# Optimization experiments

Hardware: AMD Instinct MI355X
Metric: run time of the kernel (lower is better)

Reference implementation:

```python
import jax, jax.numpy as jnp
import numpy as np

B_SZ, SEQ, CH, ORDER = 8, 8192, 256, 64
EPS_LN = 1e-5
EPS_H = 1e-6


def setup_inputs() -> dict:
    key = jax.random.key(0)
    ks = jax.random.split(key, 12)
    s = 1.0 / np.sqrt(CH)
    x = jax.random.normal(ks[0], (B_SZ, SEQ, CH), jnp.float32)
    # RTF params: A = denominator coeffs (monic, leading 1 implied), B = numerator coeffs
    A = 0.01 * jax.random.normal(ks[1], (CH, ORDER), jnp.float32)  # small -> stable 1/A(z)
    Bp = 0.1 * jax.random.normal(ks[2], (CH, ORDER), jnp.float32)
    h0 = jnp.zeros((1,), jnp.float32)  # init torch.tensor([0.])
    W_enc = s * jax.random.normal(ks[3], (CH, CH), jnp.float32)
    b_enc = jnp.zeros((CH,), jnp.float32)
    W_fc = s * jax.random.normal(ks[4], (CH, CH), jnp.float32)
    b_fc = jnp.zeros((CH,), jnp.float32)
    gamma = jnp.ones((CH,), jnp.float32)
    beta = jnp.zeros((CH,), jnp.float32)
    W_dec = s * jax.random.normal(ks[5], (CH, CH), jnp.float32)
    b_dec = jnp.zeros((CH,), jnp.float32)
    return {"x": x, "A": A, "Bp": Bp, "h0": h0, "W_enc": W_enc, "b_enc": b_enc,
            "W_fc": W_fc, "b_fc": b_fc, "gamma": gamma, "beta": beta,
            "W_dec": W_dec, "b_dec": b_dec}


def _rtf_kernel(A, Bp, L):
    # K(z) = B(z)/A(z) with monic denominator a = [1, A_1..A_order]
    C = A.shape[0]
    a = jnp.concatenate([jnp.ones((C, 1), A.dtype), A], axis=1)  # (C, order+1)
    af = jnp.fft.rfft(a, n=L, axis=1)
    bf = jnp.fft.rfft(Bp, n=L, axis=1)
    return jnp.fft.irfft(bf / af, n=L, axis=1)  # (C, L)


def _causal_fft_conv(x, K):
    # x: (B, L, C); K: (C, L) per-channel causal filter
    L = x.shape[1]
    n = 2 * L
    xf = jnp.fft.rfft(x, n=n, axis=1)            # (B, n/2+1, C)
    Kf = jnp.fft.rfft(K.T, n=n, axis=0)          # (n/2+1, C)
    return jnp.fft.irfft(xf * Kf[None], n=n, axis=1)[:, :L]


def reference(x, A, Bp, h0, W_enc, b_enc, W_fc, b_fc, gamma, beta, W_dec, b_dec):
    gelu = lambda t: jax.nn.gelu(t, approximate=False)
    xe = x @ W_enc.T + b_enc                      # encode
    L = xe.shape[1]
    K = _rtf_kernel(A, Bp, L)                     # kernel generation from (A,B)
    h1 = _causal_fft_conv(xe, K)                  # FFT long convolution
    y1 = gelu(h1 + h0 * xe)                       # SSMRTF output (mult_activation=gelu)
    y2 = gelu(y1 @ W_fc.T + b_fc)                 # fc + final_act
    y2 = y2 + xe                                  # skip
    mu = jnp.mean(y2, axis=-1, keepdims=True)     # LayerNorm over channels
    var = jnp.mean(jnp.square(y2 - mu), axis=-1, keepdims=True)
    y2 = (y2 - mu) * jax.lax.rsqrt(var + EPS_LN) * gamma + beta
    y = y2 @ W_dec.T + b_dec                      # decode
    # h = ||y||_inf over seq / ||x_enc||_inf over seq
    h = jnp.max(jnp.abs(y), axis=1) / (jnp.max(jnp.abs(xe), axis=1) + EPS_H)
    return (y, h)
```

## Files before the change

### kernel.cpp

```cpp
#include <hip/hip_runtime.h>
#include <math.h>


#define BSZ   8
#define SEQ   8192
#define CHN   256
#define ORD   64
#define STAPS 512
#define NDD   17
#define PREPAD 544
#define XROW  (PREPAD + SEQ)
#define MTOT  (BSZ * SEQ)
#define YELEMS (MTOT * CHN)

#define CT2   1024
#define CTP   1032
#define CROW2 2048

typedef short s16x8 __attribute__((ext_vector_type(8)));
typedef float f32x4 __attribute__((ext_vector_type(4)));

#define MFMA16(a, b, c) __builtin_amdgcn_mfma_f32_16x16x32_bf16((a), (b), (c), 0, 0, 0)

__device__ __forceinline__ void gll16(const void* g, void* l) {
  __builtin_amdgcn_global_load_lds(
      (const __attribute__((address_space(1))) unsigned int*)g,
      (__attribute__((address_space(3))) unsigned int*)l, 16, 0, 0);
}

#define PERMC(row, h) (((row) * 8 + ((h) ^ ((row) & 7))) * 8)

__device__ __forceinline__ unsigned short f2bf(float f) {
  unsigned u = __float_as_uint(f);
  return (unsigned short)((u + 0x7FFFu + ((u >> 16) & 1u)) >> 16);
}
__device__ __forceinline__ float bf2f(unsigned short h) {
  return __uint_as_float(((unsigned)h) << 16);
}
__device__ __forceinline__ float geluf(float x) {
  float x2 = x * x;
  float y = x * __builtin_fmaf(0.0356774081f, x2, 0.7978845608f);
  float e = __builtin_amdgcn_exp2f(-2.8853900818f * y);
  return x * __builtin_amdgcn_rcpf(1.0f + e);
}
__device__ __forceinline__ uint4 packbf8(float4 a, float4 b) {
  uint4 r;
  r.x = (unsigned)f2bf(a.x) | ((unsigned)f2bf(a.y) << 16);
  r.y = (unsigned)f2bf(a.z) | ((unsigned)f2bf(a.w) << 16);
  r.z = (unsigned)f2bf(b.x) | ((unsigned)f2bf(b.y) << 16);
  r.w = (unsigned)f2bf(b.z) | ((unsigned)f2bf(b.w) << 16);
  return r;
}

__device__ __forceinline__ void kgen8(float* smemk, const float* A, const float* Bp,
                                      unsigned short* afr, int blk) {
  int tid = threadIdx.x, lane = tid & 63, wv = tid >> 6;
  int c = blk * 8 + wv;
  float* base = smemk + wv * 1872;
  float* G0 = base;
  float* G1 = base + 584;
  float* Et = base + 1168;
  float* Asl = base + 1232;
  float* Bsl = base + 1296;
  float* Kb = base + 1360;

  Asl[lane] = A[(size_t)c * ORD + lane];
  Bsl[lane] = Bp[(size_t)c * ORD + lane];
  for (int i = lane; i < 1168; i += 64) base[i] = 0.f;
  if (lane == 0) { G0[64] = 1.f; G1[65] = 1.f; }

  for (int n = 1; n < STAPS; n <<= 1) {
    int par = (n + lane) & 1;
    const float* Gc = par ? G1 : G0;
    int I0 = 64 + n + lane + par;
    float e0 = 0.f, e1 = 0.f, e2 = 0.f, e3 = 0.f;
#pragma unroll
    for (int g = 0; g < 16; ++g) {
      float4 av = *(const float4*)&Asl[4 * g];
      float2 vA = *(const float2*)&Gc[I0 - 4 * g - 2];
      float2 vB = *(const float2*)&Gc[I0 - 4 * g - 4];
      e0 += av.x * vA.y;
      e1 += av.y * vA.x;
      e2 += av.z * vB.y;
      e3 += av.w * vB.x;
    }
    Et[lane] = (e0 + e1) + (e2 + e3);
    int nk = (n + 63) >> 6;
    for (int k = 0; k < nk; ++k) {
      int idx = k * 64 + lane;
      int parU = (idx + 1) & 1;
      const float* Gu = parU ? G1 : G0;
      int J0 = 64 + idx - 1 + parU;
      float a0 = 0.f, a1 = 0.f, a2 = 0.f, a3 = 0.f;
#pragma unroll
      for (int g = 0; g < 16; ++g) {
        float4 ev = *(const float4*)&Et[4 * g];
        float2 vA = *(const float2*)&Gu[J0 - 4 * g];
        float2 vB = *(const float2*)&Gu[J0 - 4 * g - 2];
        a0 += ev.x * vA.y;
        a1 += ev.y * vA.x;
        a2 += ev.z * vB.y;
        a3 += ev.w * vB.x;
      }
      if (idx < n) {
        float gv = -((a0 + a1) + (a2 + a3));
        G0[64 + n + idx] = gv;
        G1[65 + n + idx] = gv;
      }
    }
  }

  for (int k = 0; k < 8; ++k) {
    int t = k * 64 + lane;
    int parB = (t + 1) & 1;
    const float* Gb = parB ? G1 : G0;
    int J0 = 64 + t - 1 + parB;
    float a0 = 0.f, a1 = 0.f, a2 = 0.f, a3 = 0.f;
#pragma unroll
    for (int g = 0; g < 16; ++g) {
      float4 bv = *(const float4*)&Bsl[4 * g];
      float2 vA = *(const float2*)&Gb[J0 - 4 * g];
      float2 vB = *(const float2*)&Gb[J0 - 4 * g - 2];
      a0 += bv.x * vA.y;
      a1 += bv.y * vA.x;
      a2 += bv.z * vB.y;
      a3 += bv.w * vB.x;
    }
    Kb[t] = (a0 + a1) + (a2 + a3);
  }

  int m = lane & 15, quad = lane >> 4;
  for (int dd = 0; dd < NDD; ++dd) {
    unsigned short v[8];
#pragma unroll
    for (int j = 0; j < 8; ++j) {
      int k = quad * 8 + j;
      int d = 2 * dd + (k >> 4);
      int p = k & 15;
      int s = 16 * d + m - p;
      float kv = (s >= 0 && s < STAPS) ? Kb[s] : 0.f;
      v[j] = f2bf(kv);
    }
    uint4 pk;
    pk.x = (unsigned)v[0] | ((unsigned)v[1] << 16);
    pk.y = (unsigned)v[2] | ((unsigned)v[3] << 16);
    pk.z = (unsigned)v[4] | ((unsigned)v[5] << 16);
    pk.w = (unsigned)v[6] | ((unsigned)v[7] << 16);
    *(uint4*)(afr + ((size_t)(c * NDD + dd) * 64 + lane) * 8) = pk;
  }
}

__global__ __launch_bounds__(512) void k_pzk(const float* A, const float* Bp,
                                             unsigned short* afr,
                                             const float* we, const float* wf,
                                             const float* wd, unsigned short* owe,
                                             unsigned short* owf, unsigned short* owd,
                                             unsigned short* xeT, uint4* maxbufs) {
  __shared__ __align__(16) float smemk[8 * 1872];
  int bx = blockIdx.x, tid = threadIdx.x;
  if (bx < 32) {
    kgen8(smemk, A, Bp, afr, bx);
    return;
  }
  int i = (bx - 32) * 512 + tid;
  if (i < 196608) {
    int which = i >> 16, off = i & 65535;
    if (which == 0)      owe[off] = f2bf(we[off]);
    else if (which == 1) owf[off] = f2bf(wf[off]);
    else                 owd[off] = f2bf(wd[off]);
  } else {
    int j = i - 196608;
    uint4 z; z.x = 0; z.y = 0; z.z = 0; z.w = 0;
    if (j < 139264) {
      int row = j / 68, cc = j % 68;
      *(uint4*)((char*)xeT + (size_t)row * (XROW * 2) + (size_t)cc * 16) = z;
    } else {
      maxbufs[j - 139264] = z;
    }
  }
}

__global__ __launch_bounds__(256) void k_gemm1(const float* x, const unsigned short* wb,
                                               const float* benc, unsigned short* xeT,
                                               unsigned int* maxxe) {
  __shared__ __align__(16) char smem[40960];
  unsigned short* As = (unsigned short*)smem;
  unsigned short* Bs = (unsigned short*)(smem + 32768);
  int tid = threadIdx.x, lane = tid & 63, wv = tid >> 6;
  int ln15 = lane & 15, hf = lane >> 4;
  size_t t0 = (size_t)blockIdx.x * 64;
  int b = (int)(t0 >> 13), tin = (int)(t0 & 8191);
  f32x4 acc[4][4];
#pragma unroll
  for (int i = 0; i < 4; ++i)
#pragma unroll
    for (int j = 0; j < 4; ++j) { acc[i][j][0]=0.f; acc[i][j][1]=0.f; acc[i][j][2]=0.f; acc[i][j][3]=0.f; }

  for (int k0 = 0; k0 < CHN; k0 += 64) {
    __syncthreads();
#pragma unroll
    for (int i = 0; i < 8; ++i) {
      int p = 512 * wv + 64 * i + lane;
      int row = p >> 3, h = (p & 7) ^ (row & 7);
      gll16(wb + (size_t)row * CHN + k0 + h * 8, &As[(512 * wv + 64 * i) * 8]);
    }
    {
      int row = tid >> 2, hb = (tid & 3) * 2;
      const float* src = x + (t0 + row) * CHN + k0 + hb * 8;
      float4 f0 = *(const float4*)src;
      float4 f1 = *(const float4*)(src + 4);
      float4 f2 = *(const float4*)(src + 8);
      float4 f3 = *(const float4*)(src + 12);
      *(uint4*)&Bs[PERMC(row, hb)]     = packbf8(f0, f1);
      *(uint4*)&Bs[PERMC(row, hb + 1)] = packbf8(f2, f3);
    }
    __syncthreads();
#pragma unroll
    for (int ks = 0; ks < 2; ++ks) {
      s16x8 af[4], bfr[4];
#pragma unroll
      for (int mt = 0; mt < 4; ++mt) {
        int row = 64 * wv + 16 * mt + ln15;
        af[mt] = *(const s16x8*)&As[PERMC(row, ks * 4 + hf)];
      }
#pragma unroll
      for (int nt = 0; nt < 4; ++nt) {
        int row = 16 * nt + ln15;
        bfr[nt] = *(const s16x8*)&Bs[PERMC(row, ks * 4 + hf)];
      }
#pragma unroll
      for (int mt = 0; mt < 4; ++mt)
#pragma unroll
        for (int nt = 0; nt < 4; ++nt)
          acc[mt][nt] = MFMA16(af[mt], bfr[nt], acc[mt][nt]);
    }
  }
  int quad = hf;
  unsigned short* bb = (unsigned short*)smem;
  __syncthreads();
#pragma unroll
  for (int mt = 0; mt < 4; ++mt) {
#pragma unroll
    for (int r = 0; r < 4; ++r) {
      int row = 64 * wv + 16 * mt + 4 * quad + r;
      float bias = benc[row];
      float mv = 0.f;
#pragma unroll
      for (int nt = 0; nt < 4; ++nt) {
        float v = acc[mt][nt][r] + bias;
        bb[row * 68 + 16 * nt + ln15] = f2bf(v);
        mv = fmaxf(mv, fabsf(v));
      }
      mv = fmaxf(mv, __shfl_xor(mv, 1)); mv = fmaxf(mv, __shfl_xor(mv, 2));
      mv = fmaxf(mv, __shfl_xor(mv, 4)); mv = fmaxf(mv, __shfl_xor(mv, 8));
      if (ln15 == 0) atomicMax(&maxxe[b * CHN + row], __float_as_uint(mv));
    }
  }
  __syncthreads();
  {
    int rbase = wv * 4 + quad;
#pragma unroll
    for (int it = 0; it < 16; ++it) {
      int row = it * 16 + rbase;
      uint2 val = *(const uint2*)&bb[row * 68 + ln15 * 4];
      *(uint2*)(xeT + (size_t)(b * CHN + row) * XROW + PREPAD + tin + ln15 * 4) = val;
    }
  }
}

__global__ __launch_bounds__(512) void k_conv(const unsigned short* xeT,
                                              const unsigned short* afr,
                                              unsigned short* y1, const float* h0p) {
  __shared__ __align__(16) unsigned short xet[8 * CROW2];
  __shared__ __align__(16) unsigned short bnc[8 * CTP];
  int tid = threadIdx.x, lane = tid & 63, wv = tid >> 6;
  int idx = blockIdx.x;
  int tg = idx & 7, cg = (idx >> 3) & 31, b = idx >> 8;
  int c0 = cg * 8, t0 = tg * CT2;
  int c = c0 + wv;

  s16x8 afrg[NDD];
  {
    const unsigned short* ap = afr + (size_t)c * (NDD * 512) + (size_t)lane * 8;
#pragma unroll
    for (int dd = 0; dd < NDD; ++dd)
      afrg[dd] = *(const s16x8*)(ap + (size_t)dd * 512);
  }
  {
    int lp = lane ^ ((lane >> 3) & 7);
    const unsigned short* gbase = xeT + (size_t)(b * CHN + c) * XROW + t0;
    unsigned short* lbase = &xet[wv * CROW2];
#pragma unroll
    for (int k = 0; k < 4; ++k)
      gll16(gbase + (size_t)(64 * k + lp) * 8, &lbase[k * 64 * 8]);
  }
  float h0 = h0p[0];

  int n = lane & 15, quad = lane >> 4;
  int qc = quad - ((quad >> 1) << 2);
  const char* xb = (const char*)&xet[wv * CROW2];

  int ad[NDD];
  {
    int cb0 = 2 * n + qc + 68;
#pragma unroll
    for (int dd = 0; dd < NDD; ++dd) {
      int cc = cb0 - 4 * dd;
      ad[dd] = (cc ^ ((cc >> 3) & 7)) * 16;
    }
  }
  int ead;
  {
    int ch = 68 + 2 * n + (quad >> 1);
    ead = (ch ^ ((ch >> 3) & 7)) * 16 + 8 * (quad & 1);
  }
  __syncthreads();

#pragma unroll 1
  for (int s = 0; s < 4; ++s) {
    f32x4 a0, a1;
    a0[0]=0.f; a0[1]=0.f; a0[2]=0.f; a0[3]=0.f;
    a1[0]=0.f; a1[1]=0.f; a1[2]=0.f; a1[3]=0.f;
#pragma unroll
    for (int dd = 0; dd < 16; dd += 2) {
      a0 = MFMA16(afrg[dd],     *(const s16x8*)(xb + ad[dd]),     a0);
      a1 = MFMA16(afrg[dd + 1], *(const s16x8*)(xb + ad[dd + 1]), a1);
    }
    a0 = MFMA16(afrg[16], *(const s16x8*)(xb + ad[16]), a0);
    uint2 xvp = *(const uint2*)(xb + ead);
    unsigned short o[4];
#pragma unroll
    for (int r = 0; r < 4; ++r) {
      float xv = bf2f(((const unsigned short*)&xvp)[r]);
      float v = (a0[r] + a1[r]) + h0 * xv;
      o[r] = f2bf(geluf(v));
    }
    uint2 pw;
    pw.x = (unsigned)o[0] | ((unsigned)o[1] << 16);
    pw.y = (unsigned)o[2] | ((unsigned)o[3] << 16);
    *(uint2*)&bnc[wv * CTP + 256 * s + 16 * n + 4 * quad] = pw;
#pragma unroll
    for (int dd = 16; dd >= 8; --dd) ad[dd] = ad[dd - 8];
#pragma unroll
    for (int dd = 0; dd < 8; ++dd) ad[dd] = (ad[dd] + 512) ^ 64;
    ead = (ead + 512) ^ 64;
  }
  __syncthreads();
  {
    const size_t obase = (size_t)(b * SEQ + t0) * CHN + c0;
    int tb = tid >> 1, h = (tid & 1) * 4;
#pragma unroll
    for (int s = 0; s < 4; ++s) {
      int tl = 256 * s + tb;
      uint2 pk;
      pk.x = (unsigned)bnc[(h + 0) * CTP + tl] | ((unsigned)bnc[(h + 1) * CTP + tl] << 16);
      pk.y = (unsigned)bnc[(h + 2) * CTP + tl] | ((unsigned)bnc[(h + 3) * CTP + tl] << 16);
      *(uint2*)(y1 + obase + (size_t)tl * CHN + h) = pk;
    }
  }
}

__global__ __launch_bounds__(256) void k_gemm2(const unsigned short* y1,
                                               const unsigned short* wb, const float* bfc,
                                               const unsigned short* xeT, const float* gam,
                                               const float* bet, unsigned short* y2n) {
  __shared__ __align__(16) unsigned short Ws[256 * 64];
  __shared__ __align__(16) unsigned short Asb[64 * 64];
  __shared__ float pl[64][2][2];
  int tid = threadIdx.x, lane = tid & 63, wv = tid >> 6;
  int ln15 = lane & 15, hf = lane >> 4, quad = hf;
  size_t M0 = (size_t)blockIdx.x * 64;
  int b = (int)(M0 >> 13), tin = (int)(M0 & 8191);
  int mh = wv & 1, nh = wv >> 1;
  f32x4 acc[2][8];
#pragma unroll
  for (int i = 0; i < 2; ++i)
#pragma unroll
    for (int j = 0; j < 8; ++j) { acc[i][j][0]=0.f; acc[i][j][1]=0.f; acc[i][j][2]=0.f; acc[i][j][3]=0.f; }

  for (int k0 = 0; k0 < CHN; k0 += 64) {
    __syncthreads();
#pragma unroll
    for (int i = 0; i < 8; ++i) {
      int p = 512 * wv + 64 * i + lane;
      int row = p >> 3, h = (p & 7) ^ (row & 7);
      gll16(wb + (size_t)row * CHN + k0 + h * 8, &Ws[(512 * wv + 64 * i) * 8]);
    }
#pragma unroll
    for (int i = 0; i < 2; ++i) {
      int p = 128 * wv + 64 * i + lane;
      int row = p >> 3, h = (p & 7) ^ (row & 7);
      gll16(y1 + (M0 + row) * CHN + k0 + h * 8, &Asb[(128 * wv + 64 * i) * 8]);
    }
    __syncthreads();
#pragma unroll
    for (int ks = 0; ks < 2; ++ks) {
      s16x8 af[2], bfr[8];
#pragma unroll
      for (int mt = 0; mt < 2; ++mt) {
        int row = 32 * mh + 16 * mt + ln15;
        af[mt] = *(const s16x8*)&Asb[PERMC(row, ks * 4 + hf)];
      }
#pragma unroll
      for (int nt = 0; nt < 8; ++nt) {
        int row = 128 * nh + 16 * nt + ln15;
        bfr[nt] = *(const s16x8*)&Ws[PERMC(row, ks * 4 + hf)];
      }
#pragma unroll
      for (int mt = 0; mt < 2; ++mt)
#pragma unroll
        for (int nt = 0; nt < 8; ++nt)
          acc[mt][nt] = MFMA16(af[mt], bfr[nt], acc[mt][nt]);
    }
  }
  float g8[8], be8[8], bf8[8];
#pragma unroll
  for (int nt = 0; nt < 8; ++nt) {
    int col = 128 * nh + 16 * nt + ln15;
    g8[nt] = gam[col]; be8[nt] = bet[col]; bf8[nt] = bfc[col];
  }
#pragma unroll
  for (int mt = 0; mt < 2; ++mt) {
    int mlb = 32 * mh + 16 * mt + 4 * quad;
    uint2 xv2[8];
#pragma unroll
    for (int nt = 0; nt < 8; ++nt) {
      int col = 128 * nh + 16 * nt + ln15;
      xv2[nt] = *(const uint2*)(xeT + (size_t)(b * CHN + col) * XROW + PREPAD + tin + mlb);
    }
#pragma unroll
    for (int r = 0; r < 4; ++r) {
      int ml = mlb + r;
      float s1 = 0.f, s2 = 0.f;
#pragma unroll
      for (int nt = 0; nt < 8; ++nt) {
        float t2 = acc[mt][nt][r] + bf8[nt];
        float xv = bf2f(((const unsigned short*)&xv2[nt])[r]);
        float y2 = geluf(t2) + xv;
        acc[mt][nt][r] = y2;
        s1 += y2; s2 += y2 * y2;
      }
      s1 += __shfl_xor(s1, 1); s2 += __shfl_xor(s2, 1);
      s1 += __shfl_xor(s1, 2); s2 += __shfl_xor(s2, 2);
      s1 += __shfl_xor(s1, 4); s2 += __shfl_xor(s2, 4);
      s1 += __shfl_xor(s1, 8); s2 += __shfl_xor(s2, 8);
      if (ln15 == 0) { pl[ml][nh][0] = s1; pl[ml][nh][1] = s2; }
    }
  }
  __syncthreads();
#pragma unroll
  for (int mt = 0; mt < 2; ++mt) {
#pragma unroll
    for (int r = 0; r < 4; ++r) {
      int ml = 32 * mh + 16 * mt + 4 * quad + r;
      float s1 = pl[ml][0][0] + pl[ml][1][0];
      float s2 = pl[ml][0][1] + pl[ml][1][1];
      float mu = s1 * (1.f / 256.f);
      float var = s2 * (1.f / 256.f) - mu * mu;
      float ri = rsqrtf(var + 1e-5f);
#pragma unroll
      for (int nt = 0; nt < 8; ++nt) {
        int col = 128 * nh + 16 * nt + ln15;
        float yn = (acc[mt][nt][r] - mu) * ri * g8[nt] + be8[nt];
        y2n[(M0 + ml) * CHN + col] = f2bf(yn);
      }
    }
  }
}

__global__ __launch_bounds__(256) void k_gemm3(const unsigned short* y2n,
                                               const unsigned short* wb, const float* bd,
                                               float* yout, unsigned int* maxy) {
  __shared__ __align__(16) unsigned short Ws[256 * 64];
  __shared__ __align__(16) unsigned short Asb[64 * 64];
  int tid = threadIdx.x, lane = tid & 63, wv = tid >> 6;
  int ln15 = lane & 15, hf = lane >> 4, quad = hf;
  size_t M0 = (size_t)blockIdx.x * 64;
  int b = (int)(M0 >> 13);
  int mh = wv & 1, nh = wv >> 1;
  f32x4 acc[2][8];
#pragma unroll
  for (int i = 0; i < 2; ++i)
#pragma unroll
    for (int j = 0; j < 8; ++j) { acc[i][j][0]=0.f; acc[i][j][1]=0.f; acc[i][j][2]=0.f; acc[i][j][3]=0.f; }

  for (int k0 = 0; k0 < CHN; k0 += 64) {
    __syncthreads();
#pragma unroll
    for (int i = 0; i < 8; ++i) {
      int p = 512 * wv + 64 * i + lane;
      int row = p >> 3, h = (p & 7) ^ (row & 7);
      gll16(wb + (size_t)row * CHN + k0 + h * 8, &Ws[(512 * wv + 64 * i) * 8]);
    }
#pragma unroll
    for (int i = 0; i < 2; ++i) {
      int p = 128 * wv + 64 * i + lane;
      int row = p >> 3, h = (p & 7) ^ (row & 7);
      gll16(y2n + (M0 + row) * CHN + k0 + h * 8, &Asb[(128 * wv + 64 * i) * 8]);
    }
    __syncthreads();
#pragma unroll
    for (int ks = 0; ks < 2; ++ks) {
      s16x8 af[2], bfr[8];
#pragma unroll
      for (int mt = 0; mt < 2; ++mt) {
        int row = 32 * mh + 16 * mt + ln15;
        af[mt] = *(const s16x8*)&Asb[PERMC(row, ks * 4 + hf)];
      }
#pragma unroll
      for (int nt = 0; nt < 8; ++nt) {
        int row = 128 * nh + 16 * nt + ln15;
        bfr[nt] = *(const s16x8*)&Ws[PERMC(row, ks * 4 + hf)];
      }
#pragma unroll
      for (int mt = 0; mt < 2; ++mt)
#pragma unroll
        for (int nt = 0; nt < 8; ++nt)
          acc[mt][nt] = MFMA16(af[mt], bfr[nt], acc[mt][nt]);
    }
  }
  float bd8[8];
#pragma unroll
  for (int nt = 0; nt < 8; ++nt) bd8[nt] = bd[128 * nh + 16 * nt + ln15];
#pragma unroll
  for (int mt = 0; mt < 2; ++mt)
#pragma unroll
    for (int r = 0; r < 4; ++r) {
      int ml = 32 * mh + 16 * mt + 4 * quad + r;
#pragma unroll
      for (int nt = 0; nt < 8; ++nt) {
        int col = 128 * nh + 16 * nt + ln15;
        float v = acc[mt][nt][r] + bd8[nt];
        acc[mt][nt][r] = v;
        yout[(M0 + ml) * CHN + col] = v;
      }
    }
#pragma unroll
  for (int nt = 0; nt < 8; ++nt) {
    int col = 128 * nh + 16 * nt + ln15;
    float mv = 0.f;
#pragma unroll
    for (int mt = 0; mt < 2; ++mt)
#pragma unroll
      for (int r = 0; r < 4; ++r) mv = fmaxf(mv, fabsf(acc[mt][nt][r]));
    mv = fmaxf(mv, __shfl_xor(mv, 16));
    mv = fmaxf(mv, __shfl_xor(mv, 32));
    if (quad == 0) atomicMax(&maxy[b * CHN + col], __float_as_uint(mv));
  }
}

__global__ __launch_bounds__(256) void k_hfin(const unsigned int* maxxe,
                                              const unsigned int* maxy, float* hout) {
  int i = blockIdx.x * 256 + threadIdx.x;
  if (i < BSZ * CHN) {
    float mx = __uint_as_float(maxxe[i]);
    float my = __uint_as_float(maxy[i]);
    hout[i] = my / (mx + 1e-6f);
  }
}

extern "C" void kernel_launch(void* const* d_in, const int* in_sizes, int n_in,
                              void* d_out, int out_size, void* d_ws, size_t ws_size,
                              hipStream_t stream) {
  const float* x   = (const float*)d_in[0];
  const float* A   = (const float*)d_in[1];
  const float* Bp  = (const float*)d_in[2];
  const float* h0  = (const float*)d_in[3];
  const float* We  = (const float*)d_in[4];
  const float* be  = (const float*)d_in[5];
  const float* Wf  = (const float*)d_in[6];
  const float* bfc = (const float*)d_in[7];
  const float* gam = (const float*)d_in[8];
  const float* bet = (const float*)d_in[9];
  const float* Wd  = (const float*)d_in[10];
  const float* bd  = (const float*)d_in[11];

  char* ws = (char*)d_ws;
  unsigned short* y1  = (unsigned short*)(ws + 0);
  unsigned short* afr = (unsigned short*)(ws + 33554432);
  unsigned short* web = (unsigned short*)(ws + 38010880);
  unsigned short* wfb = (unsigned short*)(ws + 38141952);
  unsigned short* wdb = (unsigned short*)(ws + 38273024);
  unsigned int*  maxxe = (unsigned int*)(ws + 38404096);
  unsigned int*  maxy  = (unsigned int*)(ws + 38412288);

  unsigned short* xeT = (unsigned short*)d_out;
  float* yout = (float*)d_out;
  float* hout = yout + YELEMS;

  k_pzk<<<690, 512, 0, stream>>>(A, Bp, afr, We, Wf, Wd, web, wfb, wdb,
                                 xeT, (uint4*)maxxe);
  k_gemm1<<<1024, 256, 0, stream>>>(x, web, be, xeT, maxxe);
  k_conv<<<2048, 512, 0, stream>>>(xeT, afr, y1, h0);
  k_gemm2<<<1024, 256, 0, stream>>>(y1, wfb, bfc, xeT, gam, bet, y1);
  k_gemm3<<<1024, 256, 0, stream>>>(y1, wdb, bd, yout, maxy);
  k_hfin<<<8, 256, 0, stream>>>(maxxe, maxy, hout);
}
```

Baseline: 308.0 us.

## Fuse fc/LayerNorm and decode GEMMs into one kernel, move xeT to workspace

Adds k_g23, which runs the fc GEMM, GELU, skip add and LayerNorm, stages the normalized rows as bf16 in LDS, then runs the decode GEMM and max-abs reduction in the same block. This removes the y2n round trip through global memory and one kernel launch. Because yout is now written while xeT is still being read, xeT moves from the output buffer to workspace when the workspace is large enough, with the old two-kernel path kept as a fallback. gemm1 also drops its LDS-transposed store in favour of direct strided 2-byte global stores, which may coalesce worse. The fused kernel uses about 74 KB of LDS, which limits occupancy.

```diff
diff --git a/kernel.cpp b/kernel.cpp
--- a/kernel.cpp
+++ b/kernel.cpp
@@ -183,9 +183,8 @@
 __global__ __launch_bounds__(256) void k_gemm1(const float* x, const unsigned short* wb,
                                                const float* benc, unsigned short* xeT,
                                                unsigned int* maxxe) {
-  __shared__ __align__(16) char smem[40960];
-  unsigned short* As = (unsigned short*)smem;
-  unsigned short* Bs = (unsigned short*)(smem + 32768);
+  __shared__ __align__(16) unsigned short As[256 * 64];
+  __shared__ __align__(16) unsigned short Bs[64 * 64];
   int tid = threadIdx.x, lane = tid & 63, wv = tid >> 6;
   int ln15 = lane & 15, hf = lane >> 4;
   size_t t0 = (size_t)blockIdx.x * 64;
@@ -236,8 +235,6 @@
     }
   }
   int quad = hf;
-  unsigned short* bb = (unsigned short*)smem;
-  __syncthreads();
 #pragma unroll
   for (int mt = 0; mt < 4; ++mt) {
 #pragma unroll
@@ -248,22 +245,13 @@
 #pragma unroll
       for (int nt = 0; nt < 4; ++nt) {
         float v = acc[mt][nt][r] + bias;
-        bb[row * 68 + 16 * nt + ln15] = f2bf(v);
+        int t = tin + 16 * nt + ln15;
+        xeT[(size_t)(b * CHN + row) * XROW + PREPAD + t] = f2bf(v);
         mv = fmaxf(mv, fabsf(v));
       }
       mv = fmaxf(mv, __shfl_xor(mv, 1)); mv = fmaxf(mv, __shfl_xor(mv, 2));
       mv = fmaxf(mv, __shfl_xor(mv, 4)); mv = fmaxf(mv, __shfl_xor(mv, 8));
       if (ln15 == 0) atomicMax(&maxxe[b * CHN + row], __float_as_uint(mv));
-    }
-  }
-  __syncthreads();
-  {
-    int rbase = wv * 4 + quad;
-#pragma unroll
-    for (int it = 0; it < 16; ++it) {
-      int row = it * 16 + rbase;
-      uint2 val = *(const uint2*)&bb[row * 68 + ln15 * 4];
-      *(uint2*)(xeT + (size_t)(b * CHN + row) * XROW + PREPAD + tin + ln15 * 4) = val;
     }
   }
 }
@@ -357,6 +345,182 @@
       pk.y = (unsigned)bnc[(h + 2) * CTP + tl] | ((unsigned)bnc[(h + 3) * CTP + tl] << 16);
       *(uint2*)(y1 + obase + (size_t)tl * CHN + h) = pk;
     }
+  }
+}
+
+__global__ __launch_bounds__(256) void k_g23(const unsigned short* y1,
+                                             const unsigned short* wfb, const float* bfc,
+                                             const unsigned short* xeT, const float* gam,
+                                             const float* bet,
+                                             const unsigned short* wdb, const float* bd,
+                                             float* yout, unsigned int* maxy) {
+  __shared__ __align__(16) char smem[75776];
+  unsigned short* Ws  = (unsigned short*)smem;
+  unsigned short* Asb = (unsigned short*)(smem + 32768);
+  float*          pl  = (float*)(smem + 40960);
+  unsigned short* y2s = (unsigned short*)(smem + 41984);
+  int tid = threadIdx.x, lane = tid & 63, wv = tid >> 6;
+  int ln15 = lane & 15, hf = lane >> 4, quad = hf;
+  size_t M0 = (size_t)blockIdx.x * 64;
+  int b = (int)(M0 >> 13), tin = (int)(M0 & 8191);
+  int mh = wv & 1, nh = wv >> 1;
+  f32x4 acc[2][8];
+#pragma unroll
+  for (int i = 0; i < 2; ++i)
+#pragma unroll
+    for (int j = 0; j < 8; ++j) { acc[i][j][0]=0.f; acc[i][j][1]=0.f; acc[i][j][2]=0.f; acc[i][j][3]=0.f; }
+
+  for (int k0 = 0; k0 < CHN; k0 += 64) {
+    __syncthreads();
+#pragma unroll
+    for (int i = 0; i < 8; ++i) {
+      int p = 512 * wv + 64 * i + lane;
+      int row = p >> 3, h = (p & 7) ^ (row & 7);
+      gll16(wfb + (size_t)row * CHN + k0 + h * 8, &Ws[(512 * wv + 64 * i) * 8]);
+    }
+#pragma unroll
+    for (int i = 0; i < 2; ++i) {
+      int p = 128 * wv + 64 * i + lane;
+      int row = p >> 3, h = (p & 7) ^ (row & 7);
+      gll16(y1 + (M0 + row) * CHN + k0 + h * 8, &Asb[(128 * wv + 64 * i) * 8]);
+    }
+    __syncthreads();
+#pragma unroll
+    for (int ks = 0; ks < 2; ++ks) {
+      s16x8 af[2], bfr[8];
+#pragma unroll
+      for (int mt = 0; mt < 2; ++mt) {
+        int row = 32 * mh + 16 * mt + ln15;
+        af[mt] = *(const s16x8*)&Asb[PERMC(row, ks * 4 + hf)];
+      }
+#pragma unroll
+      for (int nt = 0; nt < 8; ++nt) {
+        int row = 128 * nh + 16 * nt + ln15;
+        bfr[nt] = *(const s16x8*)&Ws[PERMC(row, ks * 4 + hf)];
+      }
+#pragma unroll
+      for (int mt = 0; mt < 2; ++mt)
+#pragma unroll
+        for (int nt = 0; nt < 8; ++nt)
+          acc[mt][nt] = MFMA16(af[mt], bfr[nt], acc[mt][nt]);
+    }
+  }
+  float g8[8], be8[8], bf8[8];
+#pragma unroll
+  for (int nt = 0; nt < 8; ++nt) {
+    int col = 128 * nh + 16 * nt + ln15;
+    g8[nt] = gam[col]; be8[nt] = bet[col]; bf8[nt] = bfc[col];
+  }
+#pragma unroll
+  for (int mt = 0; mt < 2; ++mt) {
+    int mlb = 32 * mh + 16 * mt + 4 * quad;
+    uint2 xv2[8];
+#pragma unroll
+    for (int nt = 0; nt < 8; ++nt) {
+      int col = 128 * nh + 16 * nt + ln15;
+      xv2[nt] = *(const uint2*)(xeT + (size_t)(b * CHN + col) * XROW + PREPAD + tin + mlb);
+    }
+#pragma unroll
+    for (int r = 0; r < 4; ++r) {
+      int ml = mlb + r;
+      float s1 = 0.f, s2 = 0.f;
+#pragma unroll
+      for (int nt = 0; nt < 8; ++nt) {
+        float t2 = acc[mt][nt][r] + bf8[nt];
+        float xv = bf2f(((const unsigned short*)&xv2[nt])[r]);
+        float y2 = geluf(t2) + xv;
+        acc[mt][nt][r] = y2;
+        s1 += y2; s2 += y2 * y2;
+      }
+      s1 += __shfl_xor(s1, 1); s2 += __shfl_xor(s2, 1);
+      s1 += __shfl_xor(s1, 2); s2 += __shfl_xor(s2, 2);
+      s1 += __shfl_xor(s1, 4); s2 += __shfl_xor(s2, 4);
+      s1 += __shfl_xor(s1, 8); s2 += __shfl_xor(s2, 8);
+      if (ln15 == 0) { pl[(ml * 2 + nh) * 2 + 0] = s1; pl[(ml * 2 + nh) * 2 + 1] = s2; }
+    }
+  }
+  __syncthreads();
+#pragma unroll
+  for (int mt = 0; mt < 2; ++mt) {
+#pragma unroll
+    for (int r = 0; r < 4; ++r) {
+      int ml = 32 * mh + 16 * mt + 4 * quad + r;
+      float s1 = pl[(ml * 2 + 0) * 2 + 0] + pl[(ml * 2 + 1) * 2 + 0];
+      float s2 = pl[(ml * 2 + 0) * 2 + 1] + pl[(ml * 2 + 1) * 2 + 1];
+      float mu = s1 * (1.f / 256.f);
+      float var = s2 * (1.f / 256.f) - mu * mu;
+      float ri = rsqrtf(var + 1e-5f);
+#pragma unroll
+      for (int nt = 0; nt < 8; ++nt) {
+        int col = 128 * nh + 16 * nt + ln15;
+        float yn = (acc[mt][nt][r] - mu) * ri * g8[nt] + be8[nt];
+        y2s[ml * 264 + col] = f2bf(yn);
+      }
+    }
+  }
+
+  f32x4 ac2[2][8];
+#pragma unroll
+  for (int i = 0; i < 2; ++i)
+#pragma unroll
+    for (int j = 0; j < 8; ++j) { ac2[i][j][0]=0.f; ac2[i][j][1]=0.f; ac2[i][j][2]=0.f; ac2[i][j][3]=0.f; }
+
+  for (int k0 = 0; k0 < CHN; k0 += 64) {
+    __syncthreads();
+#pragma unroll
+    for (int i = 0; i < 8; ++i) {
+      int p = 512 * wv + 64 * i + lane;
+      int row = p >> 3, h = (p & 7) ^ (row & 7);
+      gll16(wdb + (size_t)row * CHN + k0 + h * 8, &Ws[(512 * wv + 64 * i) * 8]);
+    }
+    __syncthreads();
+#pragma unroll
+    for (int ks = 0; ks < 2; ++ks) {
+      s16x8 af[2], bfr[8];
+#pragma unroll
+      for (int mt = 0; mt < 2; ++mt) {
+        int row = 32 * mh + 16 * mt + ln15;
+        af[mt] = *(const s16x8*)&y2s[row * 264 + k0 + (ks * 4 + hf) * 8];
+      }
+#pragma unroll
+      for (int nt = 0; nt < 8; ++nt) {
+        int row = 128 * nh + 16 * nt + ln15;
+        bfr[nt] = *(const s16x8*)&Ws[PERMC(row, ks * 4 + hf)];
+      }
+#pragma unroll
+      for (int mt = 0; mt < 2; ++mt)
+#pragma unroll
+        for (int nt = 0; nt < 8; ++nt)
+          ac2[mt][nt] = MFMA16(af[mt], bfr[nt], ac2[mt][nt]);
+    }
+  }
+  float bd8[8];
+#pragma unroll
+  for (int nt = 0; nt < 8; ++nt) bd8[nt] = bd[128 * nh + 16 * nt + ln15];
+#pragma unroll
+  for (int mt = 0; mt < 2; ++mt)
+#pragma unroll
+    for (int r = 0; r < 4; ++r) {
+      int ml = 32 * mh + 16 * mt + 4 * quad + r;
+#pragma unroll
+      for (int nt = 0; nt < 8; ++nt) {
+        int col = 128 * nh + 16 * nt + ln15;
+        float v = ac2[mt][nt][r] + bd8[nt];
+        ac2[mt][nt][r] = v;
+        yout[(M0 + ml) * CHN + col] = v;
+      }
+    }
+#pragma unroll
+  for (int nt = 0; nt < 8; ++nt) {
+    int col = 128 * nh + 16 * nt + ln15;
+    float mv = 0.f;
+#pragma unroll
+    for (int mt = 0; mt < 2; ++mt)
+#pragma unroll
+      for (int r = 0; r < 4; ++r) mv = fmaxf(mv, fabsf(ac2[mt][nt][r]));
+    mv = fmaxf(mv, __shfl_xor(mv, 16));
+    mv = fmaxf(mv, __shfl_xor(mv, 32));
+    if (quad == 0) atomicMax(&maxy[b * CHN + col], __float_as_uint(mv));
   }
 }
 
@@ -583,16 +747,26 @@
   unsigned short* wdb = (unsigned short*)(ws + 38273024);
   unsigned int*  maxxe = (unsigned int*)(ws + 38404096);
   unsigned int*  maxy  = (unsigned int*)(ws + 38412288);
-
-  unsigned short* xeT = (unsigned short*)d_out;
+  const size_t XET_OFF = 38420480;
+  const size_t WS_NEED = XET_OFF + (size_t)2048 * XROW * 2;
+
   float* yout = (float*)d_out;
   float* hout = yout + YELEMS;
+
+  int big = (ws_size >= WS_NEED);
+  unsigned short* xeT = big ? (unsigned short*)(ws + XET_OFF)
+                            : (unsigned short*)d_out;
 
   k_pzk<<<690, 512, 0, stream>>>(A, Bp, afr, We, Wf, Wd, web, wfb, wdb,
                                  xeT, (uint4*)maxxe);
   k_gemm1<<<1024, 256, 0, stream>>>(x, web, be, xeT, maxxe);
   k_conv<<<2048, 512, 0, stream>>>(xeT, afr, y1, h0);
-  k_gemm2<<<1024, 256, 0, stream>>>(y1, wfb, bfc, xeT, gam, bet, y1);
-  k_gemm3<<<1024, 256, 0, stream>>>(y1, wdb, bd, yout, maxy);
+  if (big) {
+    k_g23<<<1024, 256, 0, stream>>>(y1, wfb, bfc, xeT, gam, bet, wdb, bd,
+                                    yout, maxy);
+  } else {
+    k_gemm2<<<1024, 256, 0, stream>>>(y1, wfb, bfc, xeT, gam, bet, y1);
+    k_gemm3<<<1024, 256, 0, stream>>>(y1, wdb, bd, yout, maxy);
+  }
   k_hfin<<<8, 256, 0, stream>>>(maxxe, maxy, hout);
 }
```

After: 323.1 us. +4.9%, slower.

## Move RTF kernel generation into encoder GEMM launch and store xe directly

Applied to the files above, without the earlier changes.

Splits the prep kernel so that weight conversion and zeroing run alone, and runs the RTF filter generation (now 4 channels per 256-thread block, 64 blocks) as extra blocks of the encoder GEMM kernel. The serial kernel-generation work can then overlap with the GEMM blocks instead of sitting in its own launch phase. It also drops the LDS-staged transpose in the GEMM epilogue and writes bf16 values straight to global memory, removing two barriers. The direct scalar 2-byte stores are less coalesced than the earlier staged uint2 writes.

```diff
diff --git a/kernel.cpp b/kernel.cpp
--- a/kernel.cpp
+++ b/kernel.cpp
@@ -52,10 +52,34 @@
   return r;
 }
 
-__device__ __forceinline__ void kgen8(float* smemk, const float* A, const float* Bp,
+__global__ __launch_bounds__(256) void k_pz(const float* we, const float* wf,
+                                            const float* wd, unsigned short* owe,
+                                            unsigned short* owf, unsigned short* owd,
+                                            unsigned short* xeT, uint4* maxbufs) {
+  int bx = blockIdx.x, tid = threadIdx.x;
+  if (bx < 768) {
+    int i = bx * 256 + tid;
+    int which = i >> 16, off = i & 65535;
+    if (which == 0)      owe[off] = f2bf(we[off]);
+    else if (which == 1) owf[off] = f2bf(wf[off]);
+    else                 owd[off] = f2bf(wd[off]);
+  } else {
+    int i = (bx - 768) * 256 + tid;
+    uint4 z; z.x = 0; z.y = 0; z.z = 0; z.w = 0;
+    if (i < 2048 * 68) {
+      int row = i / 68, cc = i % 68;
+      *(uint4*)((char*)xeT + (size_t)row * (XROW * 2) + (size_t)cc * 16) = z;
+    } else {
+      int j = i - 2048 * 68;
+      if (j < 1024) maxbufs[j] = z;
+    }
+  }
+}
+
+__device__ __forceinline__ void kgen4(float* smemk, const float* A, const float* Bp,
                                       unsigned short* afr, int blk) {
   int tid = threadIdx.x, lane = tid & 63, wv = tid >> 6;
-  int c = blk * 8 + wv;
+  int c = blk * 4 + wv;
   float* base = smemk + wv * 1872;
   float* G0 = base;
   float* G1 = base + 584;
@@ -150,45 +174,21 @@
   }
 }
 
-__global__ __launch_bounds__(512) void k_pzk(const float* A, const float* Bp,
+__global__ __launch_bounds__(256) void k_g1k(const float* A, const float* Bp,
                                              unsigned short* afr,
-                                             const float* we, const float* wf,
-                                             const float* wd, unsigned short* owe,
-                                             unsigned short* owf, unsigned short* owd,
-                                             unsigned short* xeT, uint4* maxbufs) {
-  __shared__ __align__(16) float smemk[8 * 1872];
-  int bx = blockIdx.x, tid = threadIdx.x;
-  if (bx < 32) {
-    kgen8(smemk, A, Bp, afr, bx);
+                                             const float* x, const unsigned short* wb,
+                                             const float* benc, unsigned short* xeT,
+                                             unsigned int* maxxe) {
+  __shared__ __align__(16) char smem[40960];
+  if (blockIdx.x < 64) {
+    kgen4((float*)smem, A, Bp, afr, blockIdx.x);
     return;
   }
-  int i = (bx - 32) * 512 + tid;
-  if (i < 196608) {
-    int which = i >> 16, off = i & 65535;
-    if (which == 0)      owe[off] = f2bf(we[off]);
-    else if (which == 1) owf[off] = f2bf(wf[off]);
-    else                 owd[off] = f2bf(wd[off]);
-  } else {
-    int j = i - 196608;
-    uint4 z; z.x = 0; z.y = 0; z.z = 0; z.w = 0;
-    if (j < 139264) {
-      int row = j / 68, cc = j % 68;
-      *(uint4*)((char*)xeT + (size_t)row * (XROW * 2) + (size_t)cc * 16) = z;
-    } else {
-      maxbufs[j - 139264] = z;
-    }
-  }
-}
-
-__global__ __launch_bounds__(256) void k_gemm1(const float* x, const unsigned short* wb,
-                                               const float* benc, unsigned short* xeT,
-                                               unsigned int* maxxe) {
-  __shared__ __align__(16) char smem[40960];
   unsigned short* As = (unsigned short*)smem;
   unsigned short* Bs = (unsigned short*)(smem + 32768);
   int tid = threadIdx.x, lane = tid & 63, wv = tid >> 6;
   int ln15 = lane & 15, hf = lane >> 4;
-  size_t t0 = (size_t)blockIdx.x * 64;
+  size_t t0 = (size_t)(blockIdx.x - 64) * 64;
   int b = (int)(t0 >> 13), tin = (int)(t0 & 8191);
   f32x4 acc[4][4];
 #pragma unroll
@@ -236,8 +236,6 @@
     }
   }
   int quad = hf;
-  unsigned short* bb = (unsigned short*)smem;
-  __syncthreads();
 #pragma unroll
   for (int mt = 0; mt < 4; ++mt) {
 #pragma unroll
@@ -248,22 +246,13 @@
 #pragma unroll
       for (int nt = 0; nt < 4; ++nt) {
         float v = acc[mt][nt][r] + bias;
-        bb[row * 68 + 16 * nt + ln15] = f2bf(v);
+        int t = tin + 16 * nt + ln15;
+        xeT[(size_t)(b * CHN + row) * XROW + PREPAD + t] = f2bf(v);
         mv = fmaxf(mv, fabsf(v));
       }
       mv = fmaxf(mv, __shfl_xor(mv, 1)); mv = fmaxf(mv, __shfl_xor(mv, 2));
       mv = fmaxf(mv, __shfl_xor(mv, 4)); mv = fmaxf(mv, __shfl_xor(mv, 8));
       if (ln15 == 0) atomicMax(&maxxe[b * CHN + row], __float_as_uint(mv));
-    }
-  }
-  __syncthreads();
-  {
-    int rbase = wv * 4 + quad;
-#pragma unroll
-    for (int it = 0; it < 16; ++it) {
-      int row = it * 16 + rbase;
-      uint2 val = *(const uint2*)&bb[row * 68 + ln15 * 4];
-      *(uint2*)(xeT + (size_t)(b * CHN + row) * XROW + PREPAD + tin + ln15 * 4) = val;
     }
   }
 }
@@ -588,9 +577,8 @@
   float* yout = (float*)d_out;
   float* hout = yout + YELEMS;
 
-  k_pzk<<<690, 512, 0, stream>>>(A, Bp, afr, We, Wf, Wd, web, wfb, wdb,
-                                 xeT, (uint4*)maxxe);
-  k_gemm1<<<1024, 256, 0, stream>>>(x, web, be, xeT, maxxe);
+  k_pz<<<1316, 256, 0, stream>>>(We, Wf, Wd, web, wfb, wdb, xeT, (uint4*)maxxe);
+  k_g1k<<<1088, 256, 0, stream>>>(A, Bp, afr, x, web, be, xeT, maxxe);
   k_conv<<<2048, 512, 0, stream>>>(xeT, afr, y1, h0);
   k_gemm2<<<1024, 256, 0, stream>>>(y1, wfb, bfc, xeT, gam, bet, y1);
   k_gemm3<<<1024, 256, 0, stream>>>(y1, wdb, bd, yout, maxy);
```

After: 285.7 us. -7.2%, faster.
